# Performance work log

Measured on AMD Instinct MI355X. Metric: run time of the kernel, lower is better.

Reference implementation:

```python
import jax, jax.numpy as jnp
import numpy as np

B, T, C, H = 2, 2048, 2048, 16
HD = C // H  # head dim = 128


def setup_inputs() -> dict:
    key = jax.random.key(0)
    k1, k2, k3 = jax.random.split(key, 3)
    x = jax.random.normal(k1, (B, T, C), dtype=jnp.float32)
    # torch Linear stores weight as [out_features, in_features]; y = x @ W.T
    w_attn = jax.random.normal(k2, (3 * C, C), dtype=jnp.float32) * (C ** -0.5)
    w_proj = jax.random.normal(k3, (C, C), dtype=jnp.float32) * (C ** -0.5)
    b_proj = jnp.zeros((C,), dtype=jnp.float32)
    return {"x": x, "w_attn": w_attn, "w_proj": w_proj, "b_proj": b_proj}


def reference(x, w_attn, w_proj, b_proj):
    # c_attn: [B,T,C] -> [B,T,3C], then split into q,k,v
    qkv = jnp.einsum('btc,oc->bto', x, w_attn)
    q, k, v = jnp.split(qkv, 3, axis=-1)
    # [B,T,C] -> [B,H,T,HD]
    q = q.reshape(B, T, H, HD).transpose(0, 2, 1, 3)
    k = k.reshape(B, T, H, HD).transpose(0, 2, 1, 3)
    v = v.reshape(B, T, H, HD).transpose(0, 2, 1, 3)
    scale = 1.0 / jnp.sqrt(jnp.float32(HD))
    att = jnp.einsum('bhqd,bhkd->bhqk', q, k) * scale  # [B,H,T,T]
    causal = jnp.tril(jnp.ones((T, T), dtype=bool))
    att = jnp.where(causal, att, -jnp.inf)
    att = jax.nn.softmax(att, axis=-1)
    # dropout p=0.0 (eval): identity
    y = jnp.einsum('bhqk,bhkd->bhqd', att, v)  # [B,H,T,HD]
    y = y.transpose(0, 2, 1, 3).reshape(B, T, C)
    y = jnp.einsum('btc,oc->bto', y, w_proj) + b_proj
    return y
```

## Files before the change

### kernel.cpp

```cpp
#include <hip/hip_runtime.h>
#include <hip/hip_bf16.h>
#include <stdint.h>
#include <stddef.h>

#define Bn  2
#define Tn  2048
#define Cn  2048
#define Hn  16
#define HDn 128

typedef short short8   __attribute__((ext_vector_type(8)));
typedef short short8_a __attribute__((ext_vector_type(8), may_alias));
typedef unsigned int u32x4_a __attribute__((ext_vector_type(4), may_alias));
typedef unsigned short u16x4_a __attribute__((ext_vector_type(4), may_alias));
typedef unsigned short u16x8_a __attribute__((ext_vector_type(8), may_alias));
typedef float f32x4 __attribute__((ext_vector_type(4)));

typedef __attribute__((address_space(1))) const void av1_t;
typedef __attribute__((address_space(3))) void av3_t;

__device__ inline unsigned short f2b(float f) {
    union { float f; unsigned u; } v; v.f = f;
    unsigned r = v.u + 0x7fffu + ((v.u >> 16) & 1u);
    return (unsigned short)(r >> 16);
}
__device__ inline u16x4_a cvt4_f32_bf16(u32x4_a v) {
    u16x4_a h;
#pragma unroll
    for (int e = 0; e < 4; e++) {
        unsigned u = v[e];
        unsigned r = u + 0x7fffu + ((u >> 16) & 1u);
        h[e] = (unsigned short)(r >> 16);
    }
    return h;
}

__global__ __launch_bounds__(256)
void cvt_kernel(const float* __restrict__ src, unsigned short* __restrict__ dst, int n)
{
    const int i = (blockIdx.x * 256 + threadIdx.x) * 8;
    if (i >= n) return;
    u32x4_a a = *(const u32x4_a*)((const unsigned*)src + i);
    u32x4_a b = *(const u32x4_a*)((const unsigned*)src + i + 4);
    u16x8_a o;
    u16x4_a ha = cvt4_f32_bf16(a), hb = cvt4_f32_bf16(b);
#pragma unroll
    for (int e = 0; e < 4; e++) { o[e] = ha[e]; o[e + 4] = hb[e]; }
    *(u16x8_a*)(dst + i) = o;
}

template<int OUT_F32, int HAS_BIAS>
__global__ __launch_bounds__(256)
void gemm_bb_kernel(const unsigned short* __restrict__ A,
                    const unsigned short* __restrict__ Bm,
                    const float* __restrict__ bias, void* __restrict__ Cv,
                    int M, int N, int K)
{
    __shared__ __align__(16) unsigned short As[128 * 32];
    __shared__ __align__(16) unsigned short Bs[128 * 32];

    const int tid  = threadIdx.x;
    const int lane = tid & 63;
    const int wave = tid >> 6;
    const int quad = lane >> 4;
    const int l15  = lane & 15;
    const int tm = blockIdx.x * 128;
    const int tn = blockIdx.y * 128;
    const int wr = (wave >> 1) * 64;
    const int wc = (wave & 1) * 64;

    const int srow = lane >> 2;
    const int scol = (lane & 3) * 8;

    f32x4 acc[4][4];
#pragma unroll
    for (int i = 0; i < 4; i++)
#pragma unroll
        for (int j = 0; j < 4; j++) acc[i][j] = (f32x4){0.f, 0.f, 0.f, 0.f};

    const int ksteps = K >> 5;
    for (int kt = 0; kt < ksteps; ++kt) {
        const int k0 = kt << 5;
#pragma unroll
        for (int r = 0; r < 2; r++) {
            const int row = (r * 4 + wave) * 16 + srow;
            __builtin_amdgcn_global_load_lds(
                (av1_t*)(A + (size_t)(tm + row) * K + k0 + scol),
                (av3_t*)(&As[row * 32 + scol]), 16, 0, 0);
            __builtin_amdgcn_global_load_lds(
                (av1_t*)(Bm + (size_t)(tn + row) * K + k0 + scol),
                (av3_t*)(&Bs[row * 32 + scol]), 16, 0, 0);
        }
        asm volatile("s_waitcnt vmcnt(0)" ::: "memory");
        __syncthreads();

        short8 af[4], bf[4];
#pragma unroll
        for (int i = 0; i < 4; i++)
            af[i] = (short8)(*(const short8_a*)&As[(wr + i * 16 + l15) * 32 + quad * 8]);
#pragma unroll
        for (int j = 0; j < 4; j++)
            bf[j] = (short8)(*(const short8_a*)&Bs[(wc + j * 16 + l15) * 32 + quad * 8]);
#pragma unroll
        for (int i = 0; i < 4; i++)
#pragma unroll
            for (int j = 0; j < 4; j++)
                acc[i][j] = __builtin_amdgcn_mfma_f32_16x16x32_bf16(af[i], bf[j], acc[i][j], 0, 0, 0);
        __syncthreads();
    }

#pragma unroll
    for (int i = 0; i < 4; i++) {
        const int row = tm + wr + i * 16 + quad * 4;
#pragma unroll
        for (int j = 0; j < 4; j++) {
            const int col = tn + wc + j * 16 + l15;
            const float bv = HAS_BIAS ? bias[col] : 0.0f;
#pragma unroll
            for (int r = 0; r < 4; r++) {
                if (OUT_F32)
                    ((float*)Cv)[(size_t)(row + r) * N + col] = acc[i][j][r] + bv;
                else
                    ((unsigned short*)Cv)[(size_t)(row + r) * N + col] = f2b(acc[i][j][r] + bv);
            }
        }
    }
}

#define LA0 0
#define LB0 16384
#define LA1 32768
#define LB1 49152

__global__ __launch_bounds__(512, 2)
void gemm_qkv8_kernel(const unsigned short* __restrict__ A,
                      const unsigned short* __restrict__ Bm,
                      unsigned short* __restrict__ qout,
                      unsigned short* __restrict__ kvout)
{
    __shared__ __align__(16) unsigned short lds[65536];

    const int tid  = threadIdx.x;
    const int lane = tid & 63;
    const int wave = tid >> 6;
    const int quad = lane >> 4;
    const int l15  = lane & 15;
    const int wrow = wave >> 2;
    const int wcol = wave & 3;
    const int kswz = (l15 & 4) << 2;

    const int bid = blockIdx.x;
    const int xcd = bid & 7;
    const int sl  = bid >> 3;
    const int bm  = (xcd & 1) * 8 + (sl & 7);
    const int bn  = (xcd >> 1) * 6 + (sl >> 3);
    const int tm  = bm * 256;
    const int tn  = bn * 256;

    const unsigned short* Ab = A  + (size_t)tm * Cn;
    const unsigned short* Bb = Bm + (size_t)tn * Cn;

    f32x4 acc[8][4];
#pragma unroll
    for (int i = 0; i < 8; i++)
#pragma unroll
        for (int j = 0; j < 4; j++) acc[i][j] = (f32x4){0.f, 0.f, 0.f, 0.f};

    auto stage = [&](const unsigned short* g, int kt, int base, int half) {
#pragma unroll
        for (int rr = 0; rr < 2; ++rr) {
            const int idx = rr * 512 + tid;
            const int row = idx >> 3;
            const int ks  = ((idx & 7) * 8) ^ ((row & 4) << 2);
            __builtin_amdgcn_global_load_lds(
                (av1_t*)(g + (size_t)(half * 128 + row) * Cn + kt * 64 + ks),
                (av3_t*)(lds + base + half * 8192 + idx * 8), 16, 0, 0);
        }
    };
    auto lda = [&](int base, int i, int ks) -> short8 {
        return (short8)(*(const short8_a*)&lds[base + (wrow * 128 + i * 16 + l15) * 64
                                               + ((ks * 32 + quad * 8) ^ kswz)]);
    };
    auto ldb = [&](int base, int j, int ks) -> short8 {
        return (short8)(*(const short8_a*)&lds[base + (wcol * 64 + j * 16 + l15) * 64
                                               + ((ks * 32 + quad * 8) ^ kswz)]);
    };

    stage(Ab, 0, LA0, 0); stage(Ab, 0, LA0, 1);
    stage(Bb, 0, LB0, 0); stage(Bb, 0, LB0, 1);
    stage(Ab, 1, LA1, 0); stage(Ab, 1, LA1, 1);
    asm volatile("s_waitcnt vmcnt(4)" ::: "memory");
    __builtin_amdgcn_s_barrier();

    const int nt = Cn / 64;
    for (int t = 0; t < nt; t += 2) {
        const bool tail = (t + 2 >= nt);
        short8 af[8][2], bf[2][2];

#pragma unroll
        for (int i = 0; i < 4; i++) { af[i][0] = lda(LA0, i, 0); af[i][1] = lda(LA0, i, 1); }
#pragma unroll
        for (int j = 0; j < 2; j++) { bf[j][0] = ldb(LB0, j, 0); bf[j][1] = ldb(LB0, j, 1); }
        stage(Bb, t + 1, LB1, 0);
        __builtin_amdgcn_s_barrier();
        asm volatile("s_waitcnt lgkmcnt(0)" ::: "memory");
        __builtin_amdgcn_s_setprio(1);
#pragma unroll
        for (int ks = 0; ks < 2; ks++)
#pragma unroll
            for (int i = 0; i < 4; i++)
#pragma unroll
                for (int j = 0; j < 2; j++)
                    acc[i][j] = __builtin_amdgcn_mfma_f32_16x16x32_bf16(af[i][ks], bf[j][ks], acc[i][j], 0, 0, 0);
        __builtin_amdgcn_s_setprio(0);
        __builtin_amdgcn_s_barrier();

#pragma unroll
        for (int i = 4; i < 8; i++) { af[i][0] = lda(LA0, i, 0); af[i][1] = lda(LA0, i, 1); }
        stage(Bb, t + 1, LB1, 1);
        __builtin_amdgcn_s_barrier();
        asm volatile("s_waitcnt lgkmcnt(0)" ::: "memory");
        __builtin_amdgcn_s_setprio(1);
#pragma unroll
        for (int ks = 0; ks < 2; ks++)
#pragma unroll
            for (int i = 4; i < 8; i++)
#pragma unroll
                for (int j = 0; j < 2; j++)
                    acc[i][j] = __builtin_amdgcn_mfma_f32_16x16x32_bf16(af[i][ks], bf[j][ks], acc[i][j], 0, 0, 0);
        __builtin_amdgcn_s_setprio(0);
        __builtin_amdgcn_s_barrier();

#pragma unroll
        for (int j = 0; j < 2; j++) { bf[j][0] = ldb(LB0, 2 + j, 0); bf[j][1] = ldb(LB0, 2 + j, 1); }
        if (!tail) stage(Ab, t + 2, LA0, 0);
        __builtin_amdgcn_s_barrier();
        asm volatile("s_waitcnt lgkmcnt(0)" ::: "memory");
        __builtin_amdgcn_s_setprio(1);
#pragma unroll
        for (int ks = 0; ks < 2; ks++)
#pragma unroll
            for (int i = 0; i < 4; i++)
#pragma unroll
                for (int j = 0; j < 2; j++)
                    acc[i][2 + j] = __builtin_amdgcn_mfma_f32_16x16x32_bf16(af[i][ks], bf[j][ks], acc[i][2 + j], 0, 0, 0);
        __builtin_amdgcn_s_setprio(0);
        __builtin_amdgcn_s_barrier();

        if (!tail) stage(Ab, t + 2, LA0, 1);
        __builtin_amdgcn_s_barrier();
        __builtin_amdgcn_s_setprio(1);
#pragma unroll
        for (int ks = 0; ks < 2; ks++)
#pragma unroll
            for (int i = 4; i < 8; i++)
#pragma unroll
                for (int j = 0; j < 2; j++)
                    acc[i][2 + j] = __builtin_amdgcn_mfma_f32_16x16x32_bf16(af[i][ks], bf[j][ks], acc[i][2 + j], 0, 0, 0);
        __builtin_amdgcn_s_setprio(0);
        if (tail) asm volatile("s_waitcnt vmcnt(0)" ::: "memory");
        else      asm volatile("s_waitcnt vmcnt(4)" ::: "memory");
        __builtin_amdgcn_s_barrier();

#pragma unroll
        for (int i = 0; i < 4; i++) { af[i][0] = lda(LA1, i, 0); af[i][1] = lda(LA1, i, 1); }
#pragma unroll
        for (int j = 0; j < 2; j++) { bf[j][0] = ldb(LB1, j, 0); bf[j][1] = ldb(LB1, j, 1); }
        if (!tail) stage(Bb, t + 2, LB0, 0);
        __builtin_amdgcn_s_barrier();
        asm volatile("s_waitcnt lgkmcnt(0)" ::: "memory");
        __builtin_amdgcn_s_setprio(1);
#pragma unroll
        for (int ks = 0; ks < 2; ks++)
#pragma unroll
            for (int i = 0; i < 4; i++)
#pragma unroll
                for (int j = 0; j < 2; j++)
                    acc[i][j] = __builtin_amdgcn_mfma_f32_16x16x32_bf16(af[i][ks], bf[j][ks], acc[i][j], 0, 0, 0);
        __builtin_amdgcn_s_setprio(0);
        __builtin_amdgcn_s_barrier();

#pragma unroll
        for (int i = 4; i < 8; i++) { af[i][0] = lda(LA1, i, 0); af[i][1] = lda(LA1, i, 1); }
        if (!tail) stage(Bb, t + 2, LB0, 1);
        __builtin_amdgcn_s_barrier();
        asm volatile("s_waitcnt lgkmcnt(0)" ::: "memory");
        __builtin_amdgcn_s_setprio(1);
#pragma unroll
        for (int ks = 0; ks < 2; ks++)
#pragma unroll
            for (int i = 4; i < 8; i++)
#pragma unroll
                for (int j = 0; j < 2; j++)
                    acc[i][j] = __builtin_amdgcn_mfma_f32_16x16x32_bf16(af[i][ks], bf[j][ks], acc[i][j], 0, 0, 0);
        __builtin_amdgcn_s_setprio(0);
        __builtin_amdgcn_s_barrier();

#pragma unroll
        for (int j = 0; j < 2; j++) { bf[j][0] = ldb(LB1, 2 + j, 0); bf[j][1] = ldb(LB1, 2 + j, 1); }
        if (!tail) stage(Ab, t + 3, LA1, 0);
        __builtin_amdgcn_s_barrier();
        asm volatile("s_waitcnt lgkmcnt(0)" ::: "memory");
        __builtin_amdgcn_s_setprio(1);
#pragma unroll
        for (int ks = 0; ks < 2; ks++)
#pragma unroll
            for (int i = 0; i < 4; i++)
#pragma unroll
                for (int j = 0; j < 2; j++)
                    acc[i][2 + j] = __builtin_amdgcn_mfma_f32_16x16x32_bf16(af[i][ks], bf[j][ks], acc[i][2 + j], 0, 0, 0);
        __builtin_amdgcn_s_setprio(0);
        __builtin_amdgcn_s_barrier();

        if (!tail) stage(Ab, t + 3, LA1, 1);
        __builtin_amdgcn_s_barrier();
        __builtin_amdgcn_s_setprio(1);
#pragma unroll
        for (int ks = 0; ks < 2; ks++)
#pragma unroll
            for (int i = 4; i < 8; i++)
#pragma unroll
                for (int j = 0; j < 2; j++)
                    acc[i][2 + j] = __builtin_amdgcn_mfma_f32_16x16x32_bf16(af[i][ks], bf[j][ks], acc[i][2 + j], 0, 0, 0);
        __builtin_amdgcn_s_setprio(0);
        if (tail) asm volatile("s_waitcnt vmcnt(0)" ::: "memory");
        else      asm volatile("s_waitcnt vmcnt(4)" ::: "memory");
        __builtin_amdgcn_s_barrier();
    }

    unsigned short* obase = (tn < Cn) ? qout : kvout;
    const int cofs   = (tn < Cn) ? 0 : Cn;
    const size_t ostr = (tn < Cn) ? Cn : 2 * Cn;
#pragma unroll
    for (int i = 0; i < 8; i++) {
        const int row = tm + wrow * 128 + i * 16 + quad * 4;
#pragma unroll
        for (int j = 0; j < 4; j++) {
            const int col = tn + wcol * 64 + j * 16 + l15 - cofs;
#pragma unroll
            for (int r = 0; r < 4; r++)
                obase[(size_t)(row + r) * ostr + col] = f2b(acc[i][j][r]);
        }
    }
}

__global__ __launch_bounds__(512, 2)
void attn_kernel(const unsigned short* __restrict__ q,
                 const unsigned short* __restrict__ kv,
                 unsigned short* __restrict__ outp)
{
    __shared__ __align__(16) unsigned short Ks[128 * 136];
    __shared__ __align__(16) unsigned short Vs[128 * 136];
    __shared__ __align__(16) unsigned short Ps[8][16 * 136];

    const int qp   = blockIdx.x;
    const int bh   = blockIdx.y;
    const int b    = bh >> 4;
    const int h    = bh & 15;
    const int tid  = threadIdx.x;
    const int lane = tid & 63;
    const int wave = tid >> 6;
    const int quad = lane >> 4;
    const int l15  = lane & 15;

    short8 ones;
#pragma unroll
    for (int e = 0; e < 8; e++) ones[e] = (short)0x3F80;

    for (int half = 0; half < 2; ++half) {
        const int qt = half ? (15 - qp) : qp;
        const int qrow0 = qt * 128 + wave * 16;

        short8 qf[4];
#pragma unroll
        for (int kk = 0; kk < 4; kk++) {
            const unsigned short* p = q + (size_t)(b * Tn + qrow0 + l15) * Cn
                                      + h * HDn + kk * 32 + quad * 8;
            qf[kk] = (short8)(*(const short8_a*)p);
        }

        float m_i[4], l_i[4];
        f32x4 o_acc[8];
#pragma unroll
        for (int r = 0; r < 4; r++) { m_i[r] = -1e30f; l_i[r] = 0.f; }
#pragma unroll
        for (int jd = 0; jd < 8; jd++) o_acc[jd] = (f32x4){0.f, 0.f, 0.f, 0.f};

        const int ktiles = qt + 1;

        u32x4_a kr[4], vr[4];
        auto preload = [&](int kt2) {
            const int kk0 = kt2 * 128;
#pragma unroll
            for (int rep = 0; rep < 4; ++rep) {
                const int idx  = tid + rep * 512;
                const int krow = idx >> 4;
                const int dg   = (idx & 15) * 8;
                const size_t rb = (size_t)(b * Tn + kk0 + krow) * (2 * Cn) + h * HDn + dg;
                kr[rep] = *(const u32x4_a*)(kv + rb);
                vr[rep] = *(const u32x4_a*)(kv + rb + Cn);
            }
        };
        preload(0);

        for (int kt2 = 0; kt2 < ktiles; ++kt2) {
            const int kk0 = kt2 * 128;
            __syncthreads();
#pragma unroll
            for (int rep = 0; rep < 4; ++rep) {
                const int idx  = tid + rep * 512;
                const int krow = idx >> 4;
                const int l    = idx & 15;
                const int dg   = l * 8;
                *(u32x4_a*)&Ks[krow * 136 + dg] = kr[rep];
                const int pcol = krow ^ ((l & 7) << 3);
                const unsigned short* ve = (const unsigned short*)&vr[rep];
#pragma unroll
                for (int e = 0; e < 8; e++) Vs[(dg + e) * 136 + pcol] = ve[e];
            }
            __syncthreads();
            if (kt2 + 1 < ktiles) preload(kt2 + 1);

            f32x4 s[8];
#pragma unroll
            for (int j = 0; j < 8; j++) s[j] = (f32x4){0.f, 0.f, 0.f, 0.f};
#pragma unroll
            for (int kk = 0; kk < 4; ++kk) {
                short8 kf[8];
#pragma unroll
                for (int j = 0; j < 8; j++)
                    kf[j] = (short8)(*(const short8_a*)&Ks[(j * 16 + l15) * 136 + kk * 32 + quad * 8]);
#pragma unroll
                for (int j = 0; j < 8; j++)
                    s[j] = __builtin_amdgcn_mfma_f32_16x16x32_bf16(qf[kk], kf[j], s[j], 0, 0, 0);
            }

            const bool needmask = (kk0 + 127 > qrow0);
            float alr[4];
#pragma unroll
            for (int r = 0; r < 4; r++) {
                const int qidx = qrow0 + quad * 4 + r;
                float mx = -1e30f;
#pragma unroll
                for (int j = 0; j < 8; j++) {
                    float v = s[j][r] * 0.08838834764831845f;
                    if (needmask) {
                        const int kidx = kk0 + j * 16 + l15;
                        v = (kidx <= qidx) ? v : -1e30f;
                    }
                    s[j][r] = v;
                    mx = fmaxf(mx, v);
                }
#pragma unroll
                for (int off = 1; off < 16; off <<= 1)
                    mx = fmaxf(mx, __shfl_xor(mx, off));
                const float mn = fmaxf(m_i[r], mx);
                alr[r] = __expf(fminf(m_i[r] - mn, 0.f));
                m_i[r] = mn;
#pragma unroll
                for (int j = 0; j < 8; j++) {
                    const float p = __expf(fminf(s[j][r] - mn, 0.f));
                    s[j][r] = p;
                }
#pragma unroll
                for (int jd = 0; jd < 8; jd++) o_acc[jd][r] *= alr[r];
#pragma unroll
                for (int j = 0; j < 8; j++)
                    Ps[wave][(quad * 4 + r) * 136 + j * 16 + l15] = f2b(s[j][r]);
            }
            asm volatile("s_waitcnt lgkmcnt(0)" ::: "memory");

            f32x4 lacc = (f32x4){0.f, 0.f, 0.f, 0.f};
#pragma unroll
            for (int kk2 = 0; kk2 < 4; ++kk2) {
                short8 pf = (short8)(*(const short8_a*)&Ps[wave][l15 * 136 + kk2 * 32 + quad * 8]);
#pragma unroll
                for (int jd = 0; jd < 8; jd++) {
                    const int d = jd * 16 + l15;
                    const int g = (d >> 3) & 7;
                    const int colb = ((4 * kk2 + quad) ^ g) * 8;
                    short8 vf = (short8)(*(const short8_a*)&Vs[d * 136 + colb]);
                    o_acc[jd] = __builtin_amdgcn_mfma_f32_16x16x32_bf16(pf, vf, o_acc[jd], 0, 0, 0);
                }
                lacc = __builtin_amdgcn_mfma_f32_16x16x32_bf16(pf, ones, lacc, 0, 0, 0);
            }
#pragma unroll
            for (int r = 0; r < 4; r++)
                l_i[r] = l_i[r] * alr[r] + lacc[r];
        }

#pragma unroll
        for (int r = 0; r < 4; r++) {
            const float inv = 1.0f / fmaxf(l_i[r], 1e-20f);
            const int trow = qrow0 + quad * 4 + r;
#pragma unroll
            for (int jd = 0; jd < 8; jd++) {
                const int col = h * HDn + jd * 16 + l15;
                outp[(size_t)(b * Tn + trow) * Cn + col] = f2b(o_acc[jd][r] * inv);
            }
        }
    }
}

extern "C" void kernel_launch(void* const* d_in, const int* in_sizes, int n_in,
                              void* d_out, int out_size, void* d_ws, size_t ws_size,
                              hipStream_t stream)
{
    const float* x      = (const float*)d_in[0];
    const float* w_attn = (const float*)d_in[1];
    const float* w_proj = (const float*)d_in[2];
    const float* b_proj = (const float*)d_in[3];
    float* out = (float*)d_out;

    const size_t MiB = 1024 * 1024;
    unsigned short* kvbuf = (unsigned short*)d_out;

    const int nx   = Bn * Tn * Cn;
    const int nwq  = Cn * Cn;
    const int nwkv = 2 * Cn * Cn;

    if (ws_size >= 56 * MiB) {
        unsigned short* xb   = (unsigned short*)d_ws;
        unsigned short* qbuf = (unsigned short*)((char*)d_ws + 16 * MiB);
        unsigned short* wb   = (unsigned short*)((char*)d_ws + 32 * MiB);
        const int nwa = 3 * Cn * Cn;

        cvt_kernel<<<nx / 8 / 256, 256, 0, stream>>>(x, xb, nx);
        cvt_kernel<<<nwa / 8 / 256, 256, 0, stream>>>(w_attn, wb, nwa);
        gemm_qkv8_kernel<<<dim3(384), 512, 0, stream>>>(xb, wb, qbuf, kvbuf);
        attn_kernel<<<dim3(8, Bn * Hn), 512, 0, stream>>>(qbuf, kvbuf, qbuf);
        cvt_kernel<<<nwq / 8 / 256, 256, 0, stream>>>(w_proj, wb, nwq);
        gemm_bb_kernel<1, 1><<<dim3(32, 16), 256, 0, stream>>>(qbuf, wb, b_proj, out,
                                                               Bn * Tn, Cn, Cn);
    } else {
        unsigned short* xb   = (unsigned short*)d_ws;
        unsigned short* qbuf = (unsigned short*)((char*)d_ws + 16 * MiB);
        unsigned short* wb   = (unsigned short*)((char*)d_ws + 32 * MiB);

        cvt_kernel<<<nx / 8 / 256, 256, 0, stream>>>(x, xb, nx);
        cvt_kernel<<<nwq / 8 / 256, 256, 0, stream>>>(w_attn, wb, nwq);
        gemm_bb_kernel<0, 0><<<dim3(32, 16), 256, 0, stream>>>(xb, wb, nullptr, qbuf,
                                                               Bn * Tn, Cn, Cn);
        cvt_kernel<<<nwkv / 8 / 256, 256, 0, stream>>>(w_attn + (size_t)Cn * Cn, wb, nwkv);
        gemm_bb_kernel<0, 0><<<dim3(32, 32), 256, 0, stream>>>(xb, wb, nullptr, kvbuf,
                                                               Bn * Tn, 2 * Cn, Cn);
        attn_kernel<<<dim3(8, Bn * Hn), 512, 0, stream>>>(qbuf, kvbuf, qbuf);
        cvt_kernel<<<nwq / 8 / 256, 256, 0, stream>>>(w_proj, wb, nwq);
        gemm_bb_kernel<1, 1><<<dim3(32, 16), 256, 0, stream>>>(qbuf, wb, b_proj, out,
                                                               Bn * Tn, Cn, Cn);
    }
}
```

Measured before the change: 406.4 us.

## Generalize 256x256 pipelined GEMM and use it for output projection

Templates the 8-wave 256x256 tile GEMM on the grid shape and output mode, adding an fp32-with-bias epilogue so it can replace the smaller-tile generic GEMM in the output projection. It also widens the LDS XOR swizzle from one bit to three to reduce bank conflicts on the fragment reads, and replaces the hand-tuned XCD tile mapping with a generic contiguous-chunk-per-XCD mapping. The projection now launches only 128 large blocks on a device with more CUs, so some compute units sit idle, and the new XCD mapping changes L2 locality for the QKV GEMM.

Result: faster. 394.6 us (-2.9%).

```diff
diff --git a/kernel.cpp b/kernel.cpp
--- a/kernel.cpp
+++ b/kernel.cpp
@@ -132,11 +132,14 @@
 #define LA1 32768
 #define LB1 49152
 
+template<int NBM, int NBN, int MODE>
 __global__ __launch_bounds__(512, 2)
-void gemm_qkv8_kernel(const unsigned short* __restrict__ A,
-                      const unsigned short* __restrict__ Bm,
-                      unsigned short* __restrict__ qout,
-                      unsigned short* __restrict__ kvout)
+void gemm8_kernel(const unsigned short* __restrict__ A,
+                  const unsigned short* __restrict__ Bm,
+                  const float* __restrict__ bias,
+                  unsigned short* __restrict__ qout,
+                  unsigned short* __restrict__ kvout,
+                  float* __restrict__ fout)
 {
     __shared__ __align__(16) unsigned short lds[65536];
 
@@ -147,15 +150,16 @@
     const int l15  = lane & 15;
     const int wrow = wave >> 2;
     const int wcol = wave & 3;
-    const int kswz = (l15 & 4) << 2;
-
-    const int bid = blockIdx.x;
-    const int xcd = bid & 7;
-    const int sl  = bid >> 3;
-    const int bm  = (xcd & 1) * 8 + (sl & 7);
-    const int bn  = (xcd >> 1) * 6 + (sl >> 3);
-    const int tm  = bm * 256;
-    const int tn  = bn * 256;
+    const int swz  = (l15 & 7) << 3;
+
+    const int bid  = blockIdx.x;
+    const int xcd  = bid & 7;
+    const int sl   = bid >> 3;
+    const int tile = xcd * (NBM * NBN / 8) + sl;
+    const int bm   = tile % NBM;
+    const int bn   = tile / NBM;
+    const int tm   = bm * 256;
+    const int tn   = bn * 256;
 
     const unsigned short* Ab = A  + (size_t)tm * Cn;
     const unsigned short* Bb = Bm + (size_t)tn * Cn;
@@ -171,7 +175,7 @@
         for (int rr = 0; rr < 2; ++rr) {
             const int idx = rr * 512 + tid;
             const int row = idx >> 3;
-            const int ks  = ((idx & 7) * 8) ^ ((row & 4) << 2);
+            const int ks  = ((idx & 7) * 8) ^ ((row & 7) << 3);
             __builtin_amdgcn_global_load_lds(
                 (av1_t*)(g + (size_t)(half * 128 + row) * Cn + kt * 64 + ks),
                 (av3_t*)(lds + base + half * 8192 + idx * 8), 16, 0, 0);
@@ -179,11 +183,11 @@
     };
     auto lda = [&](int base, int i, int ks) -> short8 {
         return (short8)(*(const short8_a*)&lds[base + (wrow * 128 + i * 16 + l15) * 64
-                                               + ((ks * 32 + quad * 8) ^ kswz)]);
+                                               + ((ks * 32 + quad * 8) ^ swz)]);
     };
     auto ldb = [&](int base, int j, int ks) -> short8 {
         return (short8)(*(const short8_a*)&lds[base + (wcol * 64 + j * 16 + l15) * 64
-                                               + ((ks * 32 + quad * 8) ^ kswz)]);
+                                               + ((ks * 32 + quad * 8) ^ swz)]);
     };
 
     stage(Ab, 0, LA0, 0); stage(Ab, 0, LA0, 1);
@@ -328,18 +332,34 @@
         __builtin_amdgcn_s_barrier();
     }
 
-    unsigned short* obase = (tn < Cn) ? qout : kvout;
-    const int cofs   = (tn < Cn) ? 0 : Cn;
-    const size_t ostr = (tn < Cn) ? Cn : 2 * Cn;
-#pragma unroll
-    for (int i = 0; i < 8; i++) {
-        const int row = tm + wrow * 128 + i * 16 + quad * 4;
-#pragma unroll
-        for (int j = 0; j < 4; j++) {
-            const int col = tn + wcol * 64 + j * 16 + l15 - cofs;
-#pragma unroll
-            for (int r = 0; r < 4; r++)
-                obase[(size_t)(row + r) * ostr + col] = f2b(acc[i][j][r]);
+    if (MODE == 0) {
+        unsigned short* obase = (tn < Cn) ? qout : kvout;
+        const int cofs    = (tn < Cn) ? 0 : Cn;
+        const size_t ostr = (tn < Cn) ? Cn : 2 * Cn;
+#pragma unroll
+        for (int i = 0; i < 8; i++) {
+            const int row = tm + wrow * 128 + i * 16 + quad * 4;
+#pragma unroll
+            for (int j = 0; j < 4; j++) {
+                const int col = tn + wcol * 64 + j * 16 + l15 - cofs;
+#pragma unroll
+                for (int r = 0; r < 4; r++)
+                    obase[(size_t)(row + r) * ostr + col] = f2b(acc[i][j][r]);
+            }
+        }
+    } else {
+        const int Nn = NBN * 256;
+#pragma unroll
+        for (int i = 0; i < 8; i++) {
+            const int row = tm + wrow * 128 + i * 16 + quad * 4;
+#pragma unroll
+            for (int j = 0; j < 4; j++) {
+                const int col = tn + wcol * 64 + j * 16 + l15;
+                const float bv = bias[col];
+#pragma unroll
+                for (int r = 0; r < 4; r++)
+                    fout[(size_t)(row + r) * Nn + col] = acc[i][j][r] + bv;
+            }
         }
     }
 }
@@ -527,11 +547,12 @@
 
         cvt_kernel<<<nx / 8 / 256, 256, 0, stream>>>(x, xb, nx);
         cvt_kernel<<<nwa / 8 / 256, 256, 0, stream>>>(w_attn, wb, nwa);
-        gemm_qkv8_kernel<<<dim3(384), 512, 0, stream>>>(xb, wb, qbuf, kvbuf);
+        gemm8_kernel<16, 24, 0><<<dim3(384), 512, 0, stream>>>(xb, wb, nullptr,
+                                                               qbuf, kvbuf, nullptr);
         attn_kernel<<<dim3(8, Bn * Hn), 512, 0, stream>>>(qbuf, kvbuf, qbuf);
         cvt_kernel<<<nwq / 8 / 256, 256, 0, stream>>>(w_proj, wb, nwq);
-        gemm_bb_kernel<1, 1><<<dim3(32, 16), 256, 0, stream>>>(qbuf, wb, b_proj, out,
-                                                               Bn * Tn, Cn, Cn);
+        gemm8_kernel<16, 8, 1><<<dim3(128), 512, 0, stream>>>(qbuf, wb, b_proj,
+                                                              nullptr, nullptr, out);
     } else {
         unsigned short* xb   = (unsigned short*)d_ws;
         unsigned short* qbuf = (unsigned short*)((char*)d_ws + 16 * MiB);
@@ -546,7 +567,7 @@
                                                                Bn * Tn, 2 * Cn, Cn);
         attn_kernel<<<dim3(8, Bn * Hn), 512, 0, stream>>>(qbuf, kvbuf, qbuf);
         cvt_kernel<<<nwq / 8 / 256, 256, 0, stream>>>(w_proj, wb, nwq);
-        gemm_bb_kernel<1, 1><<<dim3(32, 16), 256, 0, stream>>>(qbuf, wb, b_proj, out,
-                                                               Bn * Tn, Cn, Cn);
-    }
-}
+        gemm8_kernel<16, 8, 1><<<dim3(128), 512, 0, stream>>>(qbuf, wb, b_proj,
+                                                              nullptr, nullptr, out);
+    }
+}
```

## Retile QKV GEMM to 256x192 tiles for a 512-block grid

Applied to the files above, without the earlier changes.

Changes the fused QKV GEMM tile from 256x256 to 256x192. This gives 512 blocks instead of 384 and lets the grid divide evenly over the 256 CUs at 2 blocks per CU, removing the tail-wave imbalance. The B staging is split into thirds, the LDS footprint shrinks, the XOR swizzle widens to 8 rows, and the block-to-XCD tile mapping is recomputed. In exchange, each block reuses A data across fewer columns, and the output store adds a per-element branch between the q and kv buffers.

Measured after the change: 381.9 us. -6.0%, faster.

```diff
diff --git a/kernel.cpp b/kernel.cpp
--- a/kernel.cpp
+++ b/kernel.cpp
@@ -129,16 +129,16 @@
 
 #define LA0 0
 #define LB0 16384
-#define LA1 32768
-#define LB1 49152
+#define LA1 28672
+#define LB1 45056
 
 __global__ __launch_bounds__(512, 2)
-void gemm_qkv8_kernel(const unsigned short* __restrict__ A,
-                      const unsigned short* __restrict__ Bm,
-                      unsigned short* __restrict__ qout,
-                      unsigned short* __restrict__ kvout)
+void gemm_qkv192_kernel(const unsigned short* __restrict__ A,
+                        const unsigned short* __restrict__ Bm,
+                        unsigned short* __restrict__ qout,
+                        unsigned short* __restrict__ kvout)
 {
-    __shared__ __align__(16) unsigned short lds[65536];
+    __shared__ __align__(16) unsigned short lds[57344];
 
     const int tid  = threadIdx.x;
     const int lane = tid & 63;
@@ -147,61 +147,69 @@
     const int l15  = lane & 15;
     const int wrow = wave >> 2;
     const int wcol = wave & 3;
-    const int kswz = (l15 & 4) << 2;
-
-    const int bid = blockIdx.x;
-    const int xcd = bid & 7;
-    const int sl  = bid >> 3;
-    const int bm  = (xcd & 1) * 8 + (sl & 7);
-    const int bn  = (xcd >> 1) * 6 + (sl >> 3);
-    const int tm  = bm * 256;
-    const int tn  = bn * 256;
+    const int swz  = (l15 & 7) << 3;
+
+    const int bid  = blockIdx.x;
+    const int xcd  = bid & 7;
+    const int sl   = bid >> 3;
+    const int tile = xcd * 64 + sl;
+    const int bm   = tile & 15;
+    const int bn   = tile >> 4;
+    const int tm   = bm * 256;
+    const int tn   = bn * 192;
 
     const unsigned short* Ab = A  + (size_t)tm * Cn;
     const unsigned short* Bb = Bm + (size_t)tn * Cn;
 
-    f32x4 acc[8][4];
+    f32x4 acc[8][3];
 #pragma unroll
     for (int i = 0; i < 8; i++)
 #pragma unroll
-        for (int j = 0; j < 4; j++) acc[i][j] = (f32x4){0.f, 0.f, 0.f, 0.f};
-
-    auto stage = [&](const unsigned short* g, int kt, int base, int half) {
+        for (int j = 0; j < 3; j++) acc[i][j] = (f32x4){0.f, 0.f, 0.f, 0.f};
+
+    auto stageA = [&](int kt, int base, int half) {
 #pragma unroll
         for (int rr = 0; rr < 2; ++rr) {
             const int idx = rr * 512 + tid;
             const int row = idx >> 3;
-            const int ks  = ((idx & 7) * 8) ^ ((row & 4) << 2);
+            const int ks  = ((idx & 7) * 8) ^ ((row & 7) << 3);
             __builtin_amdgcn_global_load_lds(
-                (av1_t*)(g + (size_t)(half * 128 + row) * Cn + kt * 64 + ks),
+                (av1_t*)(Ab + (size_t)(half * 128 + row) * Cn + kt * 64 + ks),
                 (av3_t*)(lds + base + half * 8192 + idx * 8), 16, 0, 0);
         }
+    };
+    auto stageB = [&](int kt, int base, int third) {
+        const int row = third * 64 + (tid >> 3);
+        const int ks  = ((tid & 7) * 8) ^ ((row & 7) << 3);
+        __builtin_amdgcn_global_load_lds(
+            (av1_t*)(Bb + (size_t)row * Cn + kt * 64 + ks),
+            (av3_t*)(lds + base + third * 4096 + tid * 8), 16, 0, 0);
     };
     auto lda = [&](int base, int i, int ks) -> short8 {
         return (short8)(*(const short8_a*)&lds[base + (wrow * 128 + i * 16 + l15) * 64
-                                               + ((ks * 32 + quad * 8) ^ kswz)]);
+                                               + ((ks * 32 + quad * 8) ^ swz)]);
     };
     auto ldb = [&](int base, int j, int ks) -> short8 {
-        return (short8)(*(const short8_a*)&lds[base + (wcol * 64 + j * 16 + l15) * 64
-                                               + ((ks * 32 + quad * 8) ^ kswz)]);
+        return (short8)(*(const short8_a*)&lds[base + (wcol * 48 + j * 16 + l15) * 64
+                                               + ((ks * 32 + quad * 8) ^ swz)]);
     };
 
-    stage(Ab, 0, LA0, 0); stage(Ab, 0, LA0, 1);
-    stage(Bb, 0, LB0, 0); stage(Bb, 0, LB0, 1);
-    stage(Ab, 1, LA1, 0); stage(Ab, 1, LA1, 1);
+    stageA(0, LA0, 0); stageA(0, LA0, 1);
+    stageB(0, LB0, 0); stageB(0, LB0, 1); stageB(0, LB0, 2);
+    stageA(1, LA1, 0); stageA(1, LA1, 1);
     asm volatile("s_waitcnt vmcnt(4)" ::: "memory");
     __builtin_amdgcn_s_barrier();
 
     const int nt = Cn / 64;
     for (int t = 0; t < nt; t += 2) {
         const bool tail = (t + 2 >= nt);
-        short8 af[8][2], bf[2][2];
+        short8 af[8][2], bf[2][2], bf2[2];
 
 #pragma unroll
         for (int i = 0; i < 4; i++) { af[i][0] = lda(LA0, i, 0); af[i][1] = lda(LA0, i, 1); }
 #pragma unroll
         for (int j = 0; j < 2; j++) { bf[j][0] = ldb(LB0, j, 0); bf[j][1] = ldb(LB0, j, 1); }
-        stage(Bb, t + 1, LB1, 0);
+        stageB(t + 1, LB1, 0);
         __builtin_amdgcn_s_barrier();
         asm volatile("s_waitcnt lgkmcnt(0)" ::: "memory");
         __builtin_amdgcn_s_setprio(1);
@@ -217,7 +225,7 @@
 
 #pragma unroll
         for (int i = 4; i < 8; i++) { af[i][0] = lda(LA0, i, 0); af[i][1] = lda(LA0, i, 1); }
-        stage(Bb, t + 1, LB1, 1);
+        stageB(t + 1, LB1, 1);
         __builtin_amdgcn_s_barrier();
         asm volatile("s_waitcnt lgkmcnt(0)" ::: "memory");
         __builtin_amdgcn_s_setprio(1);
@@ -231,9 +239,8 @@
         __builtin_amdgcn_s_setprio(0);
         __builtin_amdgcn_s_barrier();
 
-#pragma unroll
-        for (int j = 0; j < 2; j++) { bf[j][0] = ldb(LB0, 2 + j, 0); bf[j][1] = ldb(LB0, 2 + j, 1); }
-        if (!tail) stage(Ab, t + 2, LA0, 0);
+        bf2[0] = ldb(LB0, 2, 0); bf2[1] = ldb(LB0, 2, 1);
+        stageB(t + 1, LB1, 2);
         __builtin_amdgcn_s_barrier();
         asm volatile("s_waitcnt lgkmcnt(0)" ::: "memory");
         __builtin_amdgcn_s_setprio(1);
@@ -241,22 +248,18 @@
         for (int ks = 0; ks < 2; ks++)
 #pragma unroll
             for (int i = 0; i < 4; i++)
-#pragma unroll
-                for (int j = 0; j < 2; j++)
-                    acc[i][2 + j] = __builtin_amdgcn_mfma_f32_16x16x32_bf16(af[i][ks], bf[j][ks], acc[i][2 + j], 0, 0, 0);
-        __builtin_amdgcn_s_setprio(0);
-        __builtin_amdgcn_s_barrier();
-
-        if (!tail) stage(Ab, t + 2, LA0, 1);
+                acc[i][2] = __builtin_amdgcn_mfma_f32_16x16x32_bf16(af[i][ks], bf2[ks], acc[i][2], 0, 0, 0);
+        __builtin_amdgcn_s_setprio(0);
+        __builtin_amdgcn_s_barrier();
+
+        if (!tail) { stageA(t + 2, LA0, 0); stageA(t + 2, LA0, 1); }
         __builtin_amdgcn_s_barrier();
         __builtin_amdgcn_s_setprio(1);
 #pragma unroll
         for (int ks = 0; ks < 2; ks++)
 #pragma unroll
             for (int i = 4; i < 8; i++)
-#pragma unroll
-                for (int j = 0; j < 2; j++)
-                    acc[i][2 + j] = __builtin_amdgcn_mfma_f32_16x16x32_bf16(af[i][ks], bf[j][ks], acc[i][2 + j], 0, 0, 0);
+                acc[i][2] = __builtin_amdgcn_mfma_f32_16x16x32_bf16(af[i][ks], bf2[ks], acc[i][2], 0, 0, 0);
         __builtin_amdgcn_s_setprio(0);
         if (tail) asm volatile("s_waitcnt vmcnt(0)" ::: "memory");
         else      asm volatile("s_waitcnt vmcnt(4)" ::: "memory");
@@ -266,7 +269,7 @@
         for (int i = 0; i < 4; i++) { af[i][0] = lda(LA1, i, 0); af[i][1] = lda(LA1, i, 1); }
 #pragma unroll
         for (int j = 0; j < 2; j++) { bf[j][0] = ldb(LB1, j, 0); bf[j][1] = ldb(LB1, j, 1); }
-        if (!tail) stage(Bb, t + 2, LB0, 0);
+        if (!tail) stageB(t + 2, LB0, 0);
         __builtin_amdgcn_s_barrier();
         asm volatile("s_waitcnt lgkmcnt(0)" ::: "memory");
         __builtin_amdgcn_s_setprio(1);
@@ -282,7 +285,7 @@
 
 #pragma unroll
         for (int i = 4; i < 8; i++) { af[i][0] = lda(LA1, i, 0); af[i][1] = lda(LA1, i, 1); }
-        if (!tail) stage(Bb, t + 2, LB0, 1);
+        if (!tail) stageB(t + 2, LB0, 1);
         __builtin_amdgcn_s_barrier();
         asm volatile("s_waitcnt lgkmcnt(0)" ::: "memory");
         __builtin_amdgcn_s_setprio(1);
@@ -296,9 +299,8 @@
         __builtin_amdgcn_s_setprio(0);
         __builtin_amdgcn_s_barrier();
 
-#pragma unroll
-        for (int j = 0; j < 2; j++) { bf[j][0] = ldb(LB1, 2 + j, 0); bf[j][1] = ldb(LB1, 2 + j, 1); }
-        if (!tail) stage(Ab, t + 3, LA1, 0);
+        bf2[0] = ldb(LB1, 2, 0); bf2[1] = ldb(LB1, 2, 1);
+        if (!tail) stageB(t + 2, LB0, 2);
         __builtin_amdgcn_s_barrier();
         asm volatile("s_waitcnt lgkmcnt(0)" ::: "memory");
         __builtin_amdgcn_s_setprio(1);
@@ -306,40 +308,36 @@
         for (int ks = 0; ks < 2; ks++)
 #pragma unroll
             for (int i = 0; i < 4; i++)
-#pragma unroll
-                for (int j = 0; j < 2; j++)
-                    acc[i][2 + j] = __builtin_amdgcn_mfma_f32_16x16x32_bf16(af[i][ks], bf[j][ks], acc[i][2 + j], 0, 0, 0);
-        __builtin_amdgcn_s_setprio(0);
-        __builtin_amdgcn_s_barrier();
-
-        if (!tail) stage(Ab, t + 3, LA1, 1);
+                acc[i][2] = __builtin_amdgcn_mfma_f32_16x16x32_bf16(af[i][ks], bf2[ks], acc[i][2], 0, 0, 0);
+        __builtin_amdgcn_s_setprio(0);
+        __builtin_amdgcn_s_barrier();
+
+        if (!tail) { stageA(t + 3, LA1, 0); stageA(t + 3, LA1, 1); }
         __builtin_amdgcn_s_barrier();
         __builtin_amdgcn_s_setprio(1);
 #pragma unroll
         for (int ks = 0; ks < 2; ks++)
 #pragma unroll
             for (int i = 4; i < 8; i++)
-#pragma unroll
-                for (int j = 0; j < 2; j++)
-                    acc[i][2 + j] = __builtin_amdgcn_mfma_f32_16x16x32_bf16(af[i][ks], bf[j][ks], acc[i][2 + j], 0, 0, 0);
+                acc[i][2] = __builtin_amdgcn_mfma_f32_16x16x32_bf16(af[i][ks], bf2[ks], acc[i][2], 0, 0, 0);
         __builtin_amdgcn_s_setprio(0);
         if (tail) asm volatile("s_waitcnt vmcnt(0)" ::: "memory");
         else      asm volatile("s_waitcnt vmcnt(4)" ::: "memory");
         __builtin_amdgcn_s_barrier();
     }
 
-    unsigned short* obase = (tn < Cn) ? qout : kvout;
-    const int cofs   = (tn < Cn) ? 0 : Cn;
-    const size_t ostr = (tn < Cn) ? Cn : 2 * Cn;
 #pragma unroll
     for (int i = 0; i < 8; i++) {
         const int row = tm + wrow * 128 + i * 16 + quad * 4;
 #pragma unroll
-        for (int j = 0; j < 4; j++) {
-            const int col = tn + wcol * 64 + j * 16 + l15 - cofs;
-#pragma unroll
-            for (int r = 0; r < 4; r++)
-                obase[(size_t)(row + r) * ostr + col] = f2b(acc[i][j][r]);
+        for (int j = 0; j < 3; j++) {
+            const int c = tn + wcol * 48 + j * 16 + l15;
+#pragma unroll
+            for (int r = 0; r < 4; r++) {
+                const unsigned short hb = f2b(acc[i][j][r]);
+                if (c < Cn) qout[(size_t)(row + r) * Cn + c] = hb;
+                else        kvout[(size_t)(row + r) * (2 * Cn) + (c - Cn)] = hb;
+            }
         }
     }
 }
@@ -527,7 +525,7 @@
 
         cvt_kernel<<<nx / 8 / 256, 256, 0, stream>>>(x, xb, nx);
         cvt_kernel<<<nwa / 8 / 256, 256, 0, stream>>>(w_attn, wb, nwa);
-        gemm_qkv8_kernel<<<dim3(384), 512, 0, stream>>>(xb, wb, qbuf, kvbuf);
+        gemm_qkv192_kernel<<<dim3(512), 512, 0, stream>>>(xb, wb, qbuf, kvbuf);
         attn_kernel<<<dim3(8, Bn * Hn), 512, 0, stream>>>(qbuf, kvbuf, qbuf);
         cvt_kernel<<<nwq / 8 / 256, 256, 0, stream>>>(w_proj, wb, nwq);
         gemm_bb_kernel<1, 1><<<dim3(32, 16), 256, 0, stream>>>(qbuf, wb, b_proj, out,
```
